# Performance work log

Hardware: AMD Instinct MI355X
Metric: run time of the kernel (lower is better)

The kernel has to match this reference:

```python
import jax, jax.numpy as jnp
import numpy as np

GROUP_SIZE = 128

def dequantize(imatrix, scales, zeros, group_size, out_dtype):
    # repeat group-wise scales/zeros along axis 0 to full weight shape
    rs = jnp.repeat(scales, group_size, axis=0)
    rz = jnp.repeat(zeros, group_size, axis=0)
    return ((imatrix.astype(rs.dtype) - rz.astype(rs.dtype)) * rs).astype(out_dtype)

def setup_inputs() -> dict:
    key = jax.random.key(0)
    ks = jax.random.split(key, 10)
    H, I, G = 4096, 14336, GROUP_SIZE
    B, S = 4, 2048
    x = jax.random.normal(ks[0], (B, S, H), dtype=jnp.float32)
    gate_w = jax.random.randint(ks[1], (H, I), 0, 16, dtype=jnp.int32)
    gate_z = jax.random.randint(ks[2], (H // G, I), 0, 16, dtype=jnp.int32)
    gate_s = jax.random.uniform(ks[3], (H // G, I), dtype=jnp.float32) * 0.01
    up_w = jax.random.randint(ks[4], (H, I), 0, 16, dtype=jnp.int32)
    up_z = jax.random.randint(ks[5], (H // G, I), 0, 16, dtype=jnp.int32)
    up_s = jax.random.uniform(ks[6], (H // G, I), dtype=jnp.float32) * 0.01
    down_w = jax.random.randint(ks[7], (I, H), 0, 16, dtype=jnp.int32)
    down_z = jax.random.randint(ks[8], (I // G, H), 0, 16, dtype=jnp.int32)
    down_s = jax.random.uniform(ks[9], (I // G, H), dtype=jnp.float32) * 0.01
    return {"x": x, "gate_w": gate_w, "gate_z": gate_z, "gate_s": gate_s,
            "up_w": up_w, "up_z": up_z, "up_s": up_s,
            "down_w": down_w, "down_z": down_z, "down_s": down_s}

def reference(x, gate_w, gate_z, gate_s, up_w, up_z, up_s, down_w, down_z, down_s):
    dt = x.dtype
    gate_proj = dequantize(gate_w, gate_s, gate_z, GROUP_SIZE, dt)  # [H, I]
    up_proj = dequantize(up_w, up_s, up_z, GROUP_SIZE, dt)          # [H, I]
    down_proj = dequantize(down_w, down_s, down_z, GROUP_SIZE, dt)  # [I, H]
    gate = jax.nn.silu(jnp.dot(x, gate_proj))  # [B, S, I]
    up = jnp.dot(x, up_proj)                   # [B, S, I]
    return jnp.dot(gate * up, down_proj)       # [B, S, H]
```

## Files before the change

kernel.cpp:

```cpp
#include <hip/hip_runtime.h>
#include <cstdint>
#include <cstddef>

typedef unsigned short u16;
typedef unsigned int u32;
typedef float f32x4 __attribute__((ext_vector_type(4)));
typedef __bf16 bf16x8 __attribute__((ext_vector_type(8)));

__device__ inline u16 f32_to_bf16(float f) {
  u32 u = __float_as_uint(f);
  u = (u + 0x7FFFu + ((u >> 16) & 1u)) >> 16;
  return (u16)u;
}

#define GLD16(src, dst)                                                        \
  __builtin_amdgcn_global_load_lds(                                            \
      (const __attribute__((address_space(1))) u32*)(src),                     \
      (__attribute__((address_space(3))) u32*)(dst), 16, 0, 0)

#define SBAR() __builtin_amdgcn_s_barrier()
#define SETPRIO(x) __builtin_amdgcn_s_setprio(x)
#define WAIT_LGKM0()                                                           \
  do {                                                                         \
    asm volatile("s_waitcnt lgkmcnt(0)" ::: "memory");                         \
    __builtin_amdgcn_sched_barrier(0);                                         \
  } while (0)
#define WAITV(N) asm volatile("s_waitcnt vmcnt(" #N ")" ::: "memory")
#define MFMA16(a, b, c) __builtin_amdgcn_mfma_f32_16x16x32_bf16(a, b, c, 0, 0, 0)

__device__ inline void stage_op(const char* src, void* ldsBase, int rowBase,
                                int wave) {
  GLD16(src, (char*)ldsBase + rowBase * 128 + wave * 1024);
}

__device__ inline bf16x8 fragK(const u16* tile, int row, int ks, int p) {
  const int byte = row * 128 + (((ks << 6) + (p << 4)) ^ ((row & 7) << 4));
  return *(const bf16x8*)((const char*)tile + byte);
}

__global__ void k_convert_x(const float* __restrict__ x, u16* __restrict__ o) {
  const long i = (long)blockIdx.x * 256 + threadIdx.x;
  const float4 a = ((const float4*)x)[i * 2];
  const float4 b = ((const float4*)x)[i * 2 + 1];
  uint4 r;
  r.x = (u32)f32_to_bf16(a.x) | ((u32)f32_to_bf16(a.y) << 16);
  r.y = (u32)f32_to_bf16(a.z) | ((u32)f32_to_bf16(a.w) << 16);
  r.z = (u32)f32_to_bf16(b.x) | ((u32)f32_to_bf16(b.y) << 16);
  r.w = (u32)f32_to_bf16(b.z) | ((u32)f32_to_bf16(b.w) << 16);
  ((uint4*)o)[i] = r;
}

__global__ __launch_bounds__(256) void k_dequant(const int* __restrict__ W,
                                                 const int* __restrict__ Z,
                                                 const float* __restrict__ S,
                                                 u16* __restrict__ out, int K,
                                                 int N) {
  __shared__ u16 ldsT[256 * 66];
  const int k0 = blockIdx.x * 64, n0 = blockIdx.y * 256;
  const int t = threadIdx.x;
  const int n4 = t & 63;
  const int kr = t >> 6;
  const int g = k0 >> 7;
  const int nb = n0 + n4 * 4;
  const int4 z4 = *(const int4*)(Z + (size_t)g * N + nb);
  const float4 s4 = *(const float4*)(S + (size_t)g * N + nb);
#pragma unroll
  for (int pass = 0; pass < 16; ++pass) {
    const int kl = kr + pass * 4;
    const int4 w4 = *(const int4*)(W + (size_t)(k0 + kl) * N + nb);
    ldsT[(n4 * 4 + 0) * 66 + kl] = f32_to_bf16((float)(w4.x - z4.x) * s4.x);
    ldsT[(n4 * 4 + 1) * 66 + kl] = f32_to_bf16((float)(w4.y - z4.y) * s4.y);
    ldsT[(n4 * 4 + 2) * 66 + kl] = f32_to_bf16((float)(w4.z - z4.z) * s4.z);
    ldsT[(n4 * 4 + 3) * 66 + kl] = f32_to_bf16((float)(w4.w - z4.w) * s4.w);
  }
  __syncthreads();
#pragma unroll
  for (int pass = 0; pass < 8; ++pass) {
    const int nl = pass * 32 + (t >> 3);
    const int kc = (t & 7) * 8;
    const u16* p = &ldsT[nl * 66 + kc];
    const u32 w0 = *(const u32*)(p + 0);
    const u32 w1 = *(const u32*)(p + 2);
    const u32 w2 = *(const u32*)(p + 4);
    const u32 w3 = *(const u32*)(p + 6);
    *(uint4*)(out + (size_t)(n0 + nl) * K + k0 + kc) =
        make_uint4(w0, w1, w2, w3);
  }
}

__global__ __launch_bounds__(512, 2) void k_gemm_gu(
    const u16* __restrict__ X, const u16* __restrict__ WG,
    const u16* __restrict__ WU, u16* __restrict__ Hout) {
  __shared__ __align__(16) u16 lA[2][16384];
  __shared__ __align__(16) u16 lG[2][8192];
  __shared__ __align__(16) u16 lU[2][8192];
  const int NKT = 64;
  const int m0 = blockIdx.x * 256, n0 = blockIdx.y * 128;
  const int tid = threadIdx.x, lane = tid & 63, wave = tid >> 6;
  const int p = lane >> 4, r16 = lane & 15;
  const int wr = wave >> 2, wc = wave & 3;

  const int srow = tid >> 3;
  const int skb = (((tid ^ (tid >> 3)) & 7) << 4);
  const char* baA = (const char*)X + (long)(m0 + srow) * 8192 + skb;
  const char* baG = (const char*)WG + (long)(n0 + srow) * 8192 + skb;
  const char* baU = (const char*)WU + (long)(n0 + srow) * 8192 + skb;

#define ISS_A(kt2, rb) \
  stage_op(baA + (long)(rb) * 8192 + (long)(kt2) * 128, lA[(kt2) & 1], rb, wave)
#define ISS_G(kt2, rb) \
  stage_op(baG + (long)(rb) * 8192 + (long)(kt2) * 128, lG[(kt2) & 1], rb, wave)
#define ISS_U(kt2, rb) \
  stage_op(baU + (long)(rb) * 8192 + (long)(kt2) * 128, lU[(kt2) & 1], rb, wave)

  f32x4 aG[8][2], aU[8][2];
  const f32x4 zero = {0.f, 0.f, 0.f, 0.f};
#pragma unroll
  for (int i = 0; i < 8; ++i)
#pragma unroll
    for (int j = 0; j < 2; ++j) {
      aG[i][j] = zero;
      aU[i][j] = zero;
    }

  ISS_A(0, 0); ISS_A(0, 128); ISS_G(0, 0); ISS_G(0, 64);
  ISS_U(0, 0); ISS_U(0, 64); ISS_A(0, 64); ISS_A(0, 192);
  ISS_A(1, 0); ISS_A(1, 128);
  WAITV(6);
  SBAR();

  for (int kt = 0; kt < NKT; ++kt) {
    const int b = kt & 1;
    const u16* hA = lA[b];
    const u16* hG = lG[b];
    const u16* hU = lU[b];
    bf16x8 af[2][4], gf[2][2], uf[2][2];
#pragma unroll
    for (int ks = 0; ks < 2; ++ks) {
#pragma unroll
      for (int ii = 0; ii < 4; ++ii)
        af[ks][ii] = fragK(hA, wr * 128 + ii * 16 + r16, ks, p);
#pragma unroll
      for (int j = 0; j < 2; ++j)
        gf[ks][j] = fragK(hG, wc * 32 + j * 16 + r16, ks, p);
    }
    if (kt < NKT - 1) { ISS_G(kt + 1, 0); ISS_G(kt + 1, 64); }
    SBAR();
    WAIT_LGKM0();
    SETPRIO(1);
#pragma unroll
    for (int ks = 0; ks < 2; ++ks)
#pragma unroll
      for (int ii = 0; ii < 4; ++ii)
#pragma unroll
        for (int j = 0; j < 2; ++j)
          aG[ii][j] = MFMA16(af[ks][ii], gf[ks][j], aG[ii][j]);
    SETPRIO(0);
    if (kt < NKT - 1) WAITV(6); else WAITV(2);
    SBAR();
#pragma unroll
    for (int ks = 0; ks < 2; ++ks)
#pragma unroll
      for (int j = 0; j < 2; ++j)
        uf[ks][j] = fragK(hU, wc * 32 + j * 16 + r16, ks, p);
    if (kt < NKT - 1) { ISS_U(kt + 1, 0); ISS_U(kt + 1, 64); }
    SBAR();
    WAIT_LGKM0();
    SETPRIO(1);
#pragma unroll
    for (int ks = 0; ks < 2; ++ks)
#pragma unroll
      for (int ii = 0; ii < 4; ++ii)
#pragma unroll
        for (int j = 0; j < 2; ++j)
          aU[ii][j] = MFMA16(af[ks][ii], uf[ks][j], aU[ii][j]);
    SETPRIO(0);
    if (kt < NKT - 1) WAITV(6); else WAITV(0);
    SBAR();
#pragma unroll
    for (int ks = 0; ks < 2; ++ks)
#pragma unroll
      for (int ii = 0; ii < 4; ++ii)
        af[ks][ii] = fragK(hA, wr * 128 + 64 + ii * 16 + r16, ks, p);
    if (kt < NKT - 1) { ISS_A(kt + 1, 64); ISS_A(kt + 1, 192); }
    SBAR();
    WAIT_LGKM0();
    SETPRIO(1);
#pragma unroll
    for (int ks = 0; ks < 2; ++ks)
#pragma unroll
      for (int ii = 0; ii < 4; ++ii)
#pragma unroll
        for (int j = 0; j < 2; ++j)
          aG[4 + ii][j] = MFMA16(af[ks][ii], gf[ks][j], aG[4 + ii][j]);
    SETPRIO(0);
    SBAR();
    if (kt < NKT - 2) { ISS_A(kt + 2, 0); ISS_A(kt + 2, 128); }
    SBAR();
    SETPRIO(1);
#pragma unroll
    for (int ks = 0; ks < 2; ++ks)
#pragma unroll
      for (int ii = 0; ii < 4; ++ii)
#pragma unroll
        for (int j = 0; j < 2; ++j)
          aU[4 + ii][j] = MFMA16(af[ks][ii], uf[ks][j], aU[4 + ii][j]);
    SETPRIO(0);
    if (kt < NKT - 2) WAITV(6);
    else if (kt == NKT - 2) WAITV(4);
    SBAR();
  }
#undef ISS_A
#undef ISS_G
#undef ISS_U

#pragma unroll
  for (int i = 0; i < 8; ++i) {
    const int row = m0 + wr * 128 + i * 16 + p * 4;
#pragma unroll
    for (int j = 0; j < 2; ++j) {
      const int col = n0 + wc * 32 + j * 16 + r16;
      u16* dst = Hout + (size_t)row * 14336 + col;
#pragma unroll
      for (int r = 0; r < 4; ++r) {
        const float gv = aG[i][j][r], uv = aU[i][j][r];
        const float sv = gv / (1.f + __expf(-gv)) * uv;
        dst[(size_t)r * 14336] = f32_to_bf16(sv);
      }
    }
  }
}

__global__ __launch_bounds__(512, 2) void k_gemm_down(
    const u16* __restrict__ Hin, const u16* __restrict__ WD,
    float* __restrict__ Out) {
  __shared__ __align__(16) u16 lA[2][16384];
  __shared__ __align__(16) u16 lB[2][16384];
  const int NKT = 224;
  const int m0 = blockIdx.x * 256, n0 = blockIdx.y * 256;
  const int tid = threadIdx.x, lane = tid & 63, wave = tid >> 6;
  const int p = lane >> 4, r16 = lane & 15;
  const int wr = wave >> 2, wc = wave & 3;

  const int srow = tid >> 3;
  const int skb = (((tid ^ (tid >> 3)) & 7) << 4);
  const char* baA = (const char*)Hin + (long)(m0 + srow) * 28672 + skb;
  const char* baB = (const char*)WD + (long)(n0 + srow) * 28672 + skb;

#define ISS_A(kt2, rb) \
  stage_op(baA + (long)(rb) * 28672 + (long)(kt2) * 128, lA[(kt2) & 1], rb, wave)
#define ISS_B(kt2, rb) \
  stage_op(baB + (long)(rb) * 28672 + (long)(kt2) * 128, lB[(kt2) & 1], rb, wave)

  f32x4 acc[8][4];
  const f32x4 zero = {0.f, 0.f, 0.f, 0.f};
#pragma unroll
  for (int i = 0; i < 8; ++i)
#pragma unroll
    for (int j = 0; j < 4; ++j) acc[i][j] = zero;

  ISS_A(0, 0); ISS_A(0, 128); ISS_B(0, 0); ISS_B(0, 64);
  ISS_B(0, 128); ISS_B(0, 192); ISS_A(0, 64); ISS_A(0, 192);
  ISS_A(1, 0); ISS_A(1, 128);
  WAITV(4);
  SBAR();

  for (int kt = 0; kt < NKT; ++kt) {
    const int b = kt & 1;
    const u16* hA = lA[b];
    const u16* hB = lB[b];
    bf16x8 af[2][4], bfr[2][4];
#pragma unroll
    for (int ks = 0; ks < 2; ++ks) {
#pragma unroll
      for (int ii = 0; ii < 4; ++ii)
        af[ks][ii] = fragK(hA, wr * 128 + ii * 16 + r16, ks, p);
#pragma unroll
      for (int j = 0; j < 2; ++j)
        bfr[ks][j] = fragK(hB, wc * 64 + j * 16 + r16, ks, p);
    }
    if (kt < NKT - 1) { ISS_B(kt + 1, 0); ISS_B(kt + 1, 64); }
    SBAR();
    WAIT_LGKM0();
    SETPRIO(1);
#pragma unroll
    for (int ks = 0; ks < 2; ++ks)
#pragma unroll
      for (int ii = 0; ii < 4; ++ii)
#pragma unroll
        for (int j = 0; j < 2; ++j)
          acc[ii][j] = MFMA16(af[ks][ii], bfr[ks][j], acc[ii][j]);
    SETPRIO(0);
    SBAR();
#pragma unroll
    for (int ks = 0; ks < 2; ++ks)
#pragma unroll
      for (int j = 2; j < 4; ++j)
        bfr[ks][j] = fragK(hB, wc * 64 + j * 16 + r16, ks, p);
    if (kt < NKT - 1) { ISS_B(kt + 1, 128); ISS_B(kt + 1, 192); }
    SBAR();
    WAIT_LGKM0();
    SETPRIO(1);
#pragma unroll
    for (int ks = 0; ks < 2; ++ks)
#pragma unroll
      for (int ii = 0; ii < 4; ++ii)
#pragma unroll
        for (int j = 2; j < 4; ++j)
          acc[ii][j] = MFMA16(af[ks][ii], bfr[ks][j], acc[ii][j]);
    SETPRIO(0);
    if (kt < NKT - 1) WAITV(6); else WAITV(0);
    SBAR();
#pragma unroll
    for (int ks = 0; ks < 2; ++ks)
#pragma unroll
      for (int ii = 0; ii < 4; ++ii)
        af[ks][ii] = fragK(hA, wr * 128 + 64 + ii * 16 + r16, ks, p);
    if (kt < NKT - 1) { ISS_A(kt + 1, 64); ISS_A(kt + 1, 192); }
    SBAR();
    WAIT_LGKM0();
    SETPRIO(1);
#pragma unroll
    for (int ks = 0; ks < 2; ++ks)
#pragma unroll
      for (int ii = 0; ii < 4; ++ii)
#pragma unroll
        for (int j = 0; j < 2; ++j)
          acc[4 + ii][j] = MFMA16(af[ks][ii], bfr[ks][j], acc[4 + ii][j]);
    SETPRIO(0);
    SBAR();
    if (kt < NKT - 2) { ISS_A(kt + 2, 0); ISS_A(kt + 2, 128); }
    SBAR();
    SETPRIO(1);
#pragma unroll
    for (int ks = 0; ks < 2; ++ks)
#pragma unroll
      for (int ii = 0; ii < 4; ++ii)
#pragma unroll
        for (int j = 2; j < 4; ++j)
          acc[4 + ii][j] = MFMA16(af[ks][ii], bfr[ks][j], acc[4 + ii][j]);
    SETPRIO(0);
    if (kt < NKT - 2) WAITV(4);
    else if (kt == NKT - 2) WAITV(2);
    SBAR();
  }
#undef ISS_A
#undef ISS_B

#pragma unroll
  for (int i = 0; i < 8; ++i) {
    const int row = m0 + wr * 128 + i * 16 + p * 4;
#pragma unroll
    for (int j = 0; j < 4; ++j) {
      const int col = n0 + wc * 64 + j * 16 + r16;
      float* dst = Out + (size_t)row * 4096 + col;
#pragma unroll
      for (int r = 0; r < 4; ++r) dst[(size_t)r * 4096] = acc[i][j][r];
    }
  }
}

__global__ void k_fill(float* o, long n, float v) {
  const long i = (long)blockIdx.x * 256 + threadIdx.x;
  if (i < n) o[i] = v;
}

extern "C" void kernel_launch(void* const* d_in, const int* in_sizes, int n_in,
                              void* d_out, int out_size, void* d_ws,
                              size_t ws_size, hipStream_t stream) {
  const float* x = (const float*)d_in[0];
  const int* gw = (const int*)d_in[1];
  const int* gz = (const int*)d_in[2];
  const float* gs = (const float*)d_in[3];
  const int* uw = (const int*)d_in[4];
  const int* uz = (const int*)d_in[5];
  const float* us = (const float*)d_in[6];
  const int* dw = (const int*)d_in[7];
  const int* dz = (const int*)d_in[8];
  const float* dsc = (const float*)d_in[9];
  float* out = (float*)d_out;

  const size_t NX = 33554432UL, NW = 58720256UL;
  const size_t need = 2UL * (NX + 3UL * NW + 117440512UL);
  if (ws_size < need) {
    k_fill<<<(out_size + 255) / 256, 256, 0, stream>>>(out, out_size, 1.0e6f);
    return;
  }
  u16* wsx = (u16*)d_ws;
  u16* wgq = wsx + NX;
  u16* wuq = wgq + NW;
  u16* wdq = wuq + NW;
  u16* wh = wdq + NW;

  k_convert_x<<<16384, 256, 0, stream>>>(x, wsx);
  dim3 dq1(64, 56);
  k_dequant<<<dq1, 256, 0, stream>>>(gw, gz, gs, wgq, 4096, 14336);
  k_dequant<<<dq1, 256, 0, stream>>>(uw, uz, us, wuq, 4096, 14336);
  dim3 dq2(224, 16);
  k_dequant<<<dq2, 256, 0, stream>>>(dw, dz, dsc, wdq, 14336, 4096);
  dim3 g1(32, 112);
  k_gemm_gu<<<g1, 512, 0, stream>>>(wsx, wgq, wuq, wh);
  dim3 g2(32, 16);
  k_gemm_down<<<g2, 512, 0, stream>>>(wh, wdq, out);
}
```

Before: 2.577 ms.

## Collapse GEMM main-loop phases to two per k-step with fewer barriers

Both the fused gate/up kernel and the down-projection kernel are restructured from four barrier-separated sub-phases per k-tile to two. Each wave now reads larger fragment sets up front, and the second row-half of A goes into a separate register array (ah) so its MFMAs can be grouped. Prologue load order and vmcnt wait counts are adjusted to match. The aim is to remove most s_barrier and LDS-wait stalls and give longer uninterrupted MFMA runs. The cost is higher register pressure from the extra fragment arrays, and a risk of LDS hazards now that fewer barriers guard buffer reuse.

```diff
diff --git a/kernel.cpp b/kernel.cpp
--- a/kernel.cpp
+++ b/kernel.cpp
@@ -123,10 +123,12 @@
       aU[i][j] = zero;
     }
 
-  ISS_A(0, 0); ISS_A(0, 128); ISS_G(0, 0); ISS_G(0, 64);
-  ISS_U(0, 0); ISS_U(0, 64); ISS_A(0, 64); ISS_A(0, 192);
+  ISS_A(0, 0); ISS_A(0, 128);
+  ISS_G(0, 0); ISS_G(0, 64);
+  ISS_U(0, 0); ISS_U(0, 64);
   ISS_A(1, 0); ISS_A(1, 128);
-  WAITV(6);
+  ISS_A(0, 64); ISS_A(0, 192);
+  WAITV(4);
   SBAR();
 
   for (int kt = 0; kt < NKT; ++kt) {
@@ -134,7 +136,7 @@
     const u16* hA = lA[b];
     const u16* hG = lG[b];
     const u16* hU = lU[b];
-    bf16x8 af[2][4], gf[2][2], uf[2][2];
+    bf16x8 af[2][4], gf[2][2], uf[2][2], ah[2][4];
 #pragma unroll
     for (int ks = 0; ks < 2; ++ks) {
 #pragma unroll
@@ -145,8 +147,6 @@
         gf[ks][j] = fragK(hG, wc * 32 + j * 16 + r16, ks, p);
     }
     if (kt < NKT - 1) { ISS_G(kt + 1, 0); ISS_G(kt + 1, 64); }
-    SBAR();
-    WAIT_LGKM0();
     SETPRIO(1);
 #pragma unroll
     for (int ks = 0; ks < 2; ++ks)
@@ -156,16 +156,12 @@
         for (int j = 0; j < 2; ++j)
           aG[ii][j] = MFMA16(af[ks][ii], gf[ks][j], aG[ii][j]);
     SETPRIO(0);
-    if (kt < NKT - 1) WAITV(6); else WAITV(2);
-    SBAR();
 #pragma unroll
     for (int ks = 0; ks < 2; ++ks)
 #pragma unroll
       for (int j = 0; j < 2; ++j)
         uf[ks][j] = fragK(hU, wc * 32 + j * 16 + r16, ks, p);
     if (kt < NKT - 1) { ISS_U(kt + 1, 0); ISS_U(kt + 1, 64); }
-    SBAR();
-    WAIT_LGKM0();
     SETPRIO(1);
 #pragma unroll
     for (int ks = 0; ks < 2; ++ks)
@@ -175,28 +171,16 @@
         for (int j = 0; j < 2; ++j)
           aU[ii][j] = MFMA16(af[ks][ii], uf[ks][j], aU[ii][j]);
     SETPRIO(0);
-    if (kt < NKT - 1) WAITV(6); else WAITV(0);
-    SBAR();
-#pragma unroll
-    for (int ks = 0; ks < 2; ++ks)
-#pragma unroll
-      for (int ii = 0; ii < 4; ++ii)
-        af[ks][ii] = fragK(hA, wr * 128 + 64 + ii * 16 + r16, ks, p);
-    if (kt < NKT - 1) { ISS_A(kt + 1, 64); ISS_A(kt + 1, 192); }
-    SBAR();
     WAIT_LGKM0();
-    SETPRIO(1);
-#pragma unroll
-    for (int ks = 0; ks < 2; ++ks)
-#pragma unroll
-      for (int ii = 0; ii < 4; ++ii)
-#pragma unroll
-        for (int j = 0; j < 2; ++j)
-          aG[4 + ii][j] = MFMA16(af[ks][ii], gf[ks][j], aG[4 + ii][j]);
-    SETPRIO(0);
+    if (kt < NKT - 1) WAITV(4); else WAITV(0);
     SBAR();
     if (kt < NKT - 2) { ISS_A(kt + 2, 0); ISS_A(kt + 2, 128); }
-    SBAR();
+#pragma unroll
+    for (int ks = 0; ks < 2; ++ks)
+#pragma unroll
+      for (int ii = 0; ii < 4; ++ii)
+        ah[ks][ii] = fragK(hA, wr * 128 + 64 + ii * 16 + r16, ks, p);
+    if (kt < NKT - 1) { ISS_A(kt + 1, 64); ISS_A(kt + 1, 192); }
     SETPRIO(1);
 #pragma unroll
     for (int ks = 0; ks < 2; ++ks)
@@ -204,10 +188,17 @@
       for (int ii = 0; ii < 4; ++ii)
 #pragma unroll
         for (int j = 0; j < 2; ++j)
-          aU[4 + ii][j] = MFMA16(af[ks][ii], uf[ks][j], aU[4 + ii][j]);
-    SETPRIO(0);
-    if (kt < NKT - 2) WAITV(6);
-    else if (kt == NKT - 2) WAITV(4);
+          aG[4 + ii][j] = MFMA16(ah[ks][ii], gf[ks][j], aG[4 + ii][j]);
+#pragma unroll
+    for (int ks = 0; ks < 2; ++ks)
+#pragma unroll
+      for (int ii = 0; ii < 4; ++ii)
+#pragma unroll
+        for (int j = 0; j < 2; ++j)
+          aU[4 + ii][j] = MFMA16(ah[ks][ii], uf[ks][j], aU[4 + ii][j]);
+    SETPRIO(0);
+    if (kt < NKT - 2) WAITV(4);
+    else if (kt == NKT - 2) WAITV(2);
     SBAR();
   }
 #undef ISS_A
@@ -259,9 +250,10 @@
 #pragma unroll
     for (int j = 0; j < 4; ++j) acc[i][j] = zero;
 
-  ISS_A(0, 0); ISS_A(0, 128); ISS_B(0, 0); ISS_B(0, 64);
-  ISS_B(0, 128); ISS_B(0, 192); ISS_A(0, 64); ISS_A(0, 192);
+  ISS_A(0, 0); ISS_A(0, 128);
+  ISS_B(0, 0); ISS_B(0, 64); ISS_B(0, 128); ISS_B(0, 192);
   ISS_A(1, 0); ISS_A(1, 128);
+  ISS_A(0, 64); ISS_A(0, 192);
   WAITV(4);
   SBAR();
 
@@ -269,76 +261,47 @@
     const int b = kt & 1;
     const u16* hA = lA[b];
     const u16* hB = lB[b];
-    bf16x8 af[2][4], bfr[2][4];
+    bf16x8 af[2][4], bfr[2][4], ah[2][4];
 #pragma unroll
     for (int ks = 0; ks < 2; ++ks) {
 #pragma unroll
       for (int ii = 0; ii < 4; ++ii)
         af[ks][ii] = fragK(hA, wr * 128 + ii * 16 + r16, ks, p);
 #pragma unroll
-      for (int j = 0; j < 2; ++j)
+      for (int j = 0; j < 4; ++j)
         bfr[ks][j] = fragK(hB, wc * 64 + j * 16 + r16, ks, p);
     }
-    if (kt < NKT - 1) { ISS_B(kt + 1, 0); ISS_B(kt + 1, 64); }
-    SBAR();
+    if (kt < NKT - 1) {
+      ISS_B(kt + 1, 0); ISS_B(kt + 1, 64);
+      ISS_B(kt + 1, 128); ISS_B(kt + 1, 192);
+    }
+    SETPRIO(1);
+#pragma unroll
+    for (int ks = 0; ks < 2; ++ks)
+#pragma unroll
+      for (int ii = 0; ii < 4; ++ii)
+#pragma unroll
+        for (int j = 0; j < 4; ++j)
+          acc[ii][j] = MFMA16(af[ks][ii], bfr[ks][j], acc[ii][j]);
+    SETPRIO(0);
     WAIT_LGKM0();
-    SETPRIO(1);
-#pragma unroll
-    for (int ks = 0; ks < 2; ++ks)
-#pragma unroll
-      for (int ii = 0; ii < 4; ++ii)
-#pragma unroll
-        for (int j = 0; j < 2; ++j)
-          acc[ii][j] = MFMA16(af[ks][ii], bfr[ks][j], acc[ii][j]);
-    SETPRIO(0);
-    SBAR();
-#pragma unroll
-    for (int ks = 0; ks < 2; ++ks)
-#pragma unroll
-      for (int j = 2; j < 4; ++j)
-        bfr[ks][j] = fragK(hB, wc * 64 + j * 16 + r16, ks, p);
-    if (kt < NKT - 1) { ISS_B(kt + 1, 128); ISS_B(kt + 1, 192); }
-    SBAR();
-    WAIT_LGKM0();
-    SETPRIO(1);
-#pragma unroll
-    for (int ks = 0; ks < 2; ++ks)
-#pragma unroll
-      for (int ii = 0; ii < 4; ++ii)
-#pragma unroll
-        for (int j = 2; j < 4; ++j)
-          acc[ii][j] = MFMA16(af[ks][ii], bfr[ks][j], acc[ii][j]);
-    SETPRIO(0);
-    if (kt < NKT - 1) WAITV(6); else WAITV(0);
-    SBAR();
-#pragma unroll
-    for (int ks = 0; ks < 2; ++ks)
-#pragma unroll
-      for (int ii = 0; ii < 4; ++ii)
-        af[ks][ii] = fragK(hA, wr * 128 + 64 + ii * 16 + r16, ks, p);
-    if (kt < NKT - 1) { ISS_A(kt + 1, 64); ISS_A(kt + 1, 192); }
-    SBAR();
-    WAIT_LGKM0();
-    SETPRIO(1);
-#pragma unroll
-    for (int ks = 0; ks < 2; ++ks)
-#pragma unroll
-      for (int ii = 0; ii < 4; ++ii)
-#pragma unroll
-        for (int j = 0; j < 2; ++j)
-          acc[4 + ii][j] = MFMA16(af[ks][ii], bfr[ks][j], acc[4 + ii][j]);
-    SETPRIO(0);
+    if (kt < NKT - 1) WAITV(4); else WAITV(0);
     SBAR();
     if (kt < NKT - 2) { ISS_A(kt + 2, 0); ISS_A(kt + 2, 128); }
-    SBAR();
-    SETPRIO(1);
-#pragma unroll
-    for (int ks = 0; ks < 2; ++ks)
-#pragma unroll
-      for (int ii = 0; ii < 4; ++ii)
-#pragma unroll
-        for (int j = 2; j < 4; ++j)
-          acc[4 + ii][j] = MFMA16(af[ks][ii], bfr[ks][j], acc[4 + ii][j]);
+#pragma unroll
+    for (int ks = 0; ks < 2; ++ks)
+#pragma unroll
+      for (int ii = 0; ii < 4; ++ii)
+        ah[ks][ii] = fragK(hA, wr * 128 + 64 + ii * 16 + r16, ks, p);
+    if (kt < NKT - 1) { ISS_A(kt + 1, 64); ISS_A(kt + 1, 192); }
+    SETPRIO(1);
+#pragma unroll
+    for (int ks = 0; ks < 2; ++ks)
+#pragma unroll
+      for (int ii = 0; ii < 4; ++ii)
+#pragma unroll
+        for (int j = 0; j < 4; ++j)
+          acc[4 + ii][j] = MFMA16(ah[ks][ii], bfr[ks][j], acc[4 + ii][j]);
     SETPRIO(0);
     if (kt < NKT - 2) WAITV(4);
     else if (kt == NKT - 2) WAITV(2);
```

After: 2.777 ms. +7.8%, slower.

## Make gate/up GEMM persistent over N tiles with continuous K pipeline

Applied to the files above, without the earlier changes.

The gate/up GEMM grid shrinks from 32x112 to 32x8 blocks, and each block loops over 14 N-tiles spaced 8 apart, writing the SiLU-gated output after each tile. The load pipeline runs without a break across tile boundaries, so the prologue and epilogue drain are paid once per block rather than once per tile, and the A-tile rows stay resident in L2. The grid drops to 256 blocks, which on a 256-CU device at 2 blocks per CU may leave occupancy low. The per-tile epilogue stores also stall the pipeline.

```diff
diff --git a/kernel.cpp b/kernel.cpp
--- a/kernel.cpp
+++ b/kernel.cpp
@@ -94,8 +94,9 @@
   __shared__ __align__(16) u16 lA[2][16384];
   __shared__ __align__(16) u16 lG[2][8192];
   __shared__ __align__(16) u16 lU[2][8192];
-  const int NKT = 64;
-  const int m0 = blockIdx.x * 256, n0 = blockIdx.y * 128;
+  const int NT = 896;
+  const int m0 = blockIdx.x * 256;
+  const int ng = blockIdx.y;
   const int tid = threadIdx.x, lane = tid & 63, wave = tid >> 6;
   const int p = lane >> 4, r16 = lane & 15;
   const int wr = wave >> 2, wc = wave & 3;
@@ -103,15 +104,17 @@
   const int srow = tid >> 3;
   const int skb = (((tid ^ (tid >> 3)) & 7) << 4);
   const char* baA = (const char*)X + (long)(m0 + srow) * 8192 + skb;
-  const char* baG = (const char*)WG + (long)(n0 + srow) * 8192 + skb;
-  const char* baU = (const char*)WU + (long)(n0 + srow) * 8192 + skb;
-
-#define ISS_A(kt2, rb) \
-  stage_op(baA + (long)(rb) * 8192 + (long)(kt2) * 128, lA[(kt2) & 1], rb, wave)
-#define ISS_G(kt2, rb) \
-  stage_op(baG + (long)(rb) * 8192 + (long)(kt2) * 128, lG[(kt2) & 1], rb, wave)
-#define ISS_U(kt2, rb) \
-  stage_op(baU + (long)(rb) * 8192 + (long)(kt2) * 128, lU[(kt2) & 1], rb, wave)
+  const char* baG = (const char*)WG + (long)srow * 8192 + skb;
+  const char* baU = (const char*)WU + (long)srow * 8192 + skb;
+
+#define NROW(t2) ((long)((ng + 8 * ((t2) >> 6)) << 7))
+#define KBYTE(t2) (((t2) & 63) * 128)
+#define ISS_A(t2, rb) \
+  stage_op(baA + (long)(rb) * 8192 + KBYTE(t2), lA[(t2) & 1], rb, wave)
+#define ISS_G(t2, rb) \
+  stage_op(baG + (NROW(t2) + (rb)) * 8192 + KBYTE(t2), lG[(t2) & 1], rb, wave)
+#define ISS_U(t2, rb) \
+  stage_op(baU + (NROW(t2) + (rb)) * 8192 + KBYTE(t2), lU[(t2) & 1], rb, wave)
 
   f32x4 aG[8][2], aU[8][2];
   const f32x4 zero = {0.f, 0.f, 0.f, 0.f};
@@ -129,106 +132,118 @@
   WAITV(6);
   SBAR();
 
-  for (int kt = 0; kt < NKT; ++kt) {
-    const int b = kt & 1;
-    const u16* hA = lA[b];
-    const u16* hG = lG[b];
-    const u16* hU = lU[b];
-    bf16x8 af[2][4], gf[2][2], uf[2][2];
-#pragma unroll
-    for (int ks = 0; ks < 2; ++ks) {
-#pragma unroll
-      for (int ii = 0; ii < 4; ++ii)
-        af[ks][ii] = fragK(hA, wr * 128 + ii * 16 + r16, ks, p);
-#pragma unroll
-      for (int j = 0; j < 2; ++j)
-        gf[ks][j] = fragK(hG, wc * 32 + j * 16 + r16, ks, p);
+  for (int r = 0; r < 14; ++r) {
+    for (int kt = 0; kt < 64; ++kt) {
+      const int t = r * 64 + kt;
+      const int b = kt & 1;
+      const u16* hA = lA[b];
+      const u16* hG = lG[b];
+      const u16* hU = lU[b];
+      bf16x8 af[2][4], gf[2][2], uf[2][2];
+#pragma unroll
+      for (int ks = 0; ks < 2; ++ks) {
+#pragma unroll
+        for (int ii = 0; ii < 4; ++ii)
+          af[ks][ii] = fragK(hA, wr * 128 + ii * 16 + r16, ks, p);
+#pragma unroll
+        for (int j = 0; j < 2; ++j)
+          gf[ks][j] = fragK(hG, wc * 32 + j * 16 + r16, ks, p);
+      }
+      if (t < NT - 1) { ISS_G(t + 1, 0); ISS_G(t + 1, 64); }
+      SBAR();
+      WAIT_LGKM0();
+      SETPRIO(1);
+#pragma unroll
+      for (int ks = 0; ks < 2; ++ks)
+#pragma unroll
+        for (int ii = 0; ii < 4; ++ii)
+#pragma unroll
+          for (int j = 0; j < 2; ++j)
+            aG[ii][j] = MFMA16(af[ks][ii], gf[ks][j], aG[ii][j]);
+      SETPRIO(0);
+      if (t < NT - 1) WAITV(6); else WAITV(2);
+      SBAR();
+#pragma unroll
+      for (int ks = 0; ks < 2; ++ks)
+#pragma unroll
+        for (int j = 0; j < 2; ++j)
+          uf[ks][j] = fragK(hU, wc * 32 + j * 16 + r16, ks, p);
+      if (t < NT - 1) { ISS_U(t + 1, 0); ISS_U(t + 1, 64); }
+      SBAR();
+      WAIT_LGKM0();
+      SETPRIO(1);
+#pragma unroll
+      for (int ks = 0; ks < 2; ++ks)
+#pragma unroll
+        for (int ii = 0; ii < 4; ++ii)
+#pragma unroll
+          for (int j = 0; j < 2; ++j)
+            aU[ii][j] = MFMA16(af[ks][ii], uf[ks][j], aU[ii][j]);
+      SETPRIO(0);
+      if (t < NT - 1) WAITV(6); else WAITV(0);
+      SBAR();
+#pragma unroll
+      for (int ks = 0; ks < 2; ++ks)
+#pragma unroll
+        for (int ii = 0; ii < 4; ++ii)
+          af[ks][ii] = fragK(hA, wr * 128 + 64 + ii * 16 + r16, ks, p);
+      if (t < NT - 1) { ISS_A(t + 1, 64); ISS_A(t + 1, 192); }
+      SBAR();
+      WAIT_LGKM0();
+      SETPRIO(1);
+#pragma unroll
+      for (int ks = 0; ks < 2; ++ks)
+#pragma unroll
+        for (int ii = 0; ii < 4; ++ii)
+#pragma unroll
+          for (int j = 0; j < 2; ++j)
+            aG[4 + ii][j] = MFMA16(af[ks][ii], gf[ks][j], aG[4 + ii][j]);
+      SETPRIO(0);
+      SBAR();
+      if (t < NT - 2) { ISS_A(t + 2, 0); ISS_A(t + 2, 128); }
+      SBAR();
+      SETPRIO(1);
+#pragma unroll
+      for (int ks = 0; ks < 2; ++ks)
+#pragma unroll
+        for (int ii = 0; ii < 4; ++ii)
+#pragma unroll
+          for (int j = 0; j < 2; ++j)
+            aU[4 + ii][j] = MFMA16(af[ks][ii], uf[ks][j], aU[4 + ii][j]);
+      SETPRIO(0);
+      if (t < NT - 2) WAITV(6);
+      else if (t == NT - 2) WAITV(4);
+      SBAR();
     }
-    if (kt < NKT - 1) { ISS_G(kt + 1, 0); ISS_G(kt + 1, 64); }
-    SBAR();
-    WAIT_LGKM0();
-    SETPRIO(1);
-#pragma unroll
-    for (int ks = 0; ks < 2; ++ks)
-#pragma unroll
-      for (int ii = 0; ii < 4; ++ii)
-#pragma unroll
-        for (int j = 0; j < 2; ++j)
-          aG[ii][j] = MFMA16(af[ks][ii], gf[ks][j], aG[ii][j]);
-    SETPRIO(0);
-    if (kt < NKT - 1) WAITV(6); else WAITV(2);
-    SBAR();
-#pragma unroll
-    for (int ks = 0; ks < 2; ++ks)
-#pragma unroll
-      for (int j = 0; j < 2; ++j)
-        uf[ks][j] = fragK(hU, wc * 32 + j * 16 + r16, ks, p);
-    if (kt < NKT - 1) { ISS_U(kt + 1, 0); ISS_U(kt + 1, 64); }
-    SBAR();
-    WAIT_LGKM0();
-    SETPRIO(1);
-#pragma unroll
-    for (int ks = 0; ks < 2; ++ks)
-#pragma unroll
-      for (int ii = 0; ii < 4; ++ii)
-#pragma unroll
-        for (int j = 0; j < 2; ++j)
-          aU[ii][j] = MFMA16(af[ks][ii], uf[ks][j], aU[ii][j]);
-    SETPRIO(0);
-    if (kt < NKT - 1) WAITV(6); else WAITV(0);
-    SBAR();
-#pragma unroll
-    for (int ks = 0; ks < 2; ++ks)
-#pragma unroll
-      for (int ii = 0; ii < 4; ++ii)
-        af[ks][ii] = fragK(hA, wr * 128 + 64 + ii * 16 + r16, ks, p);
-    if (kt < NKT - 1) { ISS_A(kt + 1, 64); ISS_A(kt + 1, 192); }
-    SBAR();
-    WAIT_LGKM0();
-    SETPRIO(1);
-#pragma unroll
-    for (int ks = 0; ks < 2; ++ks)
-#pragma unroll
-      for (int ii = 0; ii < 4; ++ii)
-#pragma unroll
-        for (int j = 0; j < 2; ++j)
-          aG[4 + ii][j] = MFMA16(af[ks][ii], gf[ks][j], aG[4 + ii][j]);
-    SETPRIO(0);
-    SBAR();
-    if (kt < NKT - 2) { ISS_A(kt + 2, 0); ISS_A(kt + 2, 128); }
-    SBAR();
-    SETPRIO(1);
-#pragma unroll
-    for (int ks = 0; ks < 2; ++ks)
-#pragma unroll
-      for (int ii = 0; ii < 4; ++ii)
-#pragma unroll
-        for (int j = 0; j < 2; ++j)
-          aU[4 + ii][j] = MFMA16(af[ks][ii], uf[ks][j], aU[4 + ii][j]);
-    SETPRIO(0);
-    if (kt < NKT - 2) WAITV(6);
-    else if (kt == NKT - 2) WAITV(4);
-    SBAR();
+    const int n0 = (ng + 8 * r) << 7;
+#pragma unroll
+    for (int i = 0; i < 8; ++i) {
+      const int row = m0 + wr * 128 + i * 16 + p * 4;
+#pragma unroll
+      for (int j = 0; j < 2; ++j) {
+        const int col = n0 + wc * 32 + j * 16 + r16;
+        u16* dst = Hout + (size_t)row * 14336 + col;
+#pragma unroll
+        for (int rr = 0; rr < 4; ++rr) {
+          const float gv = aG[i][j][rr], uv = aU[i][j][rr];
+          const float sv = gv / (1.f + __expf(-gv)) * uv;
+          dst[(size_t)rr * 14336] = f32_to_bf16(sv);
+        }
+      }
+    }
+#pragma unroll
+    for (int i = 0; i < 8; ++i)
+#pragma unroll
+      for (int j = 0; j < 2; ++j) {
+        aG[i][j] = zero;
+        aU[i][j] = zero;
+      }
   }
 #undef ISS_A
 #undef ISS_G
 #undef ISS_U
-
-#pragma unroll
-  for (int i = 0; i < 8; ++i) {
-    const int row = m0 + wr * 128 + i * 16 + p * 4;
-#pragma unroll
-    for (int j = 0; j < 2; ++j) {
-      const int col = n0 + wc * 32 + j * 16 + r16;
-      u16* dst = Hout + (size_t)row * 14336 + col;
-#pragma unroll
-      for (int r = 0; r < 4; ++r) {
-        const float gv = aG[i][j][r], uv = aU[i][j][r];
-        const float sv = gv / (1.f + __expf(-gv)) * uv;
-        dst[(size_t)r * 14336] = f32_to_bf16(sv);
-      }
-    }
-  }
+#undef NROW
+#undef KBYTE
 }
 
 __global__ __launch_bounds__(512, 2) void k_gemm_down(
@@ -398,7 +413,7 @@
   k_dequant<<<dq1, 256, 0, stream>>>(uw, uz, us, wuq, 4096, 14336);
   dim3 dq2(224, 16);
   k_dequant<<<dq2, 256, 0, stream>>>(dw, dz, dsc, wdq, 14336, 4096);
-  dim3 g1(32, 112);
+  dim3 g1(32, 8);
   k_gemm_gu<<<g1, 512, 0, stream>>>(wsx, wgq, wuq, wh);
   dim3 g2(32, 16);
   k_gemm_down<<<g2, 512, 0, stream>>>(wh, wdq, out);
```

Result: slower. 2.688 ms (+4.3%).
